# Kernel optimization log

Measured on AMD Instinct MI355X. Metric: run time of the kernel, lower is better.

The kernel has to match this reference:

```python
import jax, jax.numpy as jnp
import numpy as np

N_WIRES = 5
TOTAL = 2 * N_WIRES          # query branch simulates 2*n_wires qubits
DIM = 1 << TOTAL             # 1024
ENC = 1 << N_WIRES           # 32 = token encoder output dim


def setup_inputs() -> dict:
    key = jax.random.key(0)
    ks = jax.random.split(key, 6)
    B, T, C = 4, 32, 512
    x = jax.random.normal(ks[0], (B, T, C), jnp.float32)
    W_tok = jax.random.normal(ks[1], (ENC, C), jnp.float32) * 0.05
    b_tok = jax.random.normal(ks[2], (ENC,), jnp.float32) * 0.05
    theta_rx0 = jax.random.normal(ks[3], (TOTAL,), jnp.float32)
    theta_ry0 = jax.random.normal(ks[4], (TOTAL,), jnp.float32)
    theta_ry1 = jax.random.normal(ks[5], (TOTAL,), jnp.float32)
    return {"x": x, "W_tok": W_tok, "b_tok": b_tok,
            "theta_rx0": theta_rx0, "theta_ry0": theta_ry0, "theta_ry1": theta_ry1}


def _rx_mat(t):
    c = jnp.cos(t / 2).astype(jnp.complex64)
    s = jnp.sin(t / 2).astype(jnp.complex64)
    return jnp.stack([jnp.stack([c, -1j * s]), jnp.stack([-1j * s, c])])


def _ry_mat(t):
    c = jnp.cos(t / 2).astype(jnp.complex64)
    s = jnp.sin(t / 2).astype(jnp.complex64)
    return jnp.stack([jnp.stack([c, -s]), jnp.stack([s, c])])


def _apply_1q(state, U, w):
    # state: (bsz, 2, 2, ..., 2); wire w lives on axis 1+w (wire 0 = MSB)
    s = jnp.tensordot(state, U, axes=((1 + w,), (1,)))  # gate axis moves to last
    return jnp.moveaxis(s, -1, 1 + w)


def _apply_cnot(state, c, t):
    s = jnp.moveaxis(state, (1 + c, 1 + t), (-2, -1))
    s = s.at[..., 1, :].set(s[..., 1, ::-1])  # flip target where control == 1
    return jnp.moveaxis(s, (-2, -1), (1 + c, 1 + t))


def reference(x, W_tok, b_tok, theta_rx0, theta_ry0, theta_ry1):
    B, T, C = x.shape
    # token encoding + L2 normalize  -> (B, T, 32)
    enc = x @ W_tok.T + b_tok
    enc = enc / jnp.linalg.norm(enc, axis=-1, keepdims=True)
    # all T*T pairwise outer products, flattened as a_idx*32 + b_idx  -> (B, T*T, 1024)
    pairs = jnp.einsum('bip,bjq->bijpq', enc, enc).reshape(B, T * T, DIM)
    pairs = pairs / jnp.linalg.norm(pairs, axis=-1, keepdims=True)
    state = pairs.astype(jnp.complex64).reshape((B * T * T,) + (2,) * TOTAL)
    # layer 1: RX then RY on every wire
    for j in range(TOTAL):
        state = _apply_1q(state, _rx_mat(theta_rx0[j]), j)
        state = _apply_1q(state, _ry_mat(theta_ry0[j]), j)
    # CNOT ring
    for j in range(TOTAL):
        state = _apply_cnot(state, j, (j + 1) % TOTAL)
    # layer 2: RY on every wire
    for j in range(TOTAL):
        state = _apply_1q(state, _ry_mat(theta_ry1[j]), j)
    return state.reshape(B, T * T, DIM)
```

## Files before the change

### kernel.cpp

```cpp
#include <hip/hip_runtime.h>
#include <hip/hip_bf16.h>


typedef float vfloat4 __attribute__((ext_vector_type(4)));

__device__ __forceinline__ float2 shflx(float2 v, int mask) {
    return make_float2(__shfl_xor(v.x, mask, 64), __shfl_xor(v.y, mask, 64));
}

__global__ __launch_bounds__(256) void prep_kernel(const float* __restrict__ x,
                                                   const float* __restrict__ W,
                                                   const float* __restrict__ bt,
                                                   const float* __restrict__ rx0,
                                                   const float* __restrict__ ry0,
                                                   const float* __restrict__ ry1,
                                                   float2* __restrict__ U,
                                                   float2* __restrict__ V) {
    int row = blockIdx.x;
    int tid = threadIdx.x;

    __shared__ float g1[10][8];
    __shared__ float g2[10][2];
    __shared__ float esum[32];
    __shared__ float e[32];

    if (tid < 10) {
        float sx, cx, s0, c0, s1, c1;
        sincosf(rx0[tid] * 0.5f, &sx, &cx);
        sincosf(ry0[tid] * 0.5f, &s0, &c0);
        sincosf(ry1[tid] * 0.5f, &s1, &c1);
        g1[tid][0] = c0 * cx;  g1[tid][1] = s0 * sx;
        g1[tid][2] = -s0 * cx; g1[tid][3] = -c0 * sx;
        g1[tid][4] = s0 * cx;  g1[tid][5] = -c0 * sx;
        g1[tid][6] = c0 * cx;  g1[tid][7] = -s0 * sx;
        g2[tid][0] = c1;       g2[tid][1] = s1;
    }

    {
        int col = tid >> 3;
        int kk  = tid & 7;
        const float4* wp = (const float4*)(W + (size_t)col * 512 + kk * 4);
        const float4* xp = (const float4*)(x + (size_t)row * 512 + kk * 4);
        float acc = 0.f;
#pragma unroll
        for (int m = 0; m < 16; ++m) {
            float4 wv = wp[m * 8];
            float4 xv = xp[m * 8];
            acc += xv.x * wv.x + xv.y * wv.y + xv.z * wv.z + xv.w * wv.w;
        }
        acc += __shfl_xor(acc, 1, 64);
        acc += __shfl_xor(acc, 2, 64);
        acc += __shfl_xor(acc, 4, 64);
        if (kk == 0) esum[col] = acc;
    }
    __syncthreads();

    if (tid < 32) {
        float sum = esum[tid] + bt[tid];
        float sq = sum * sum;
#pragma unroll
        for (int off = 1; off < 32; off <<= 1) sq += __shfl_xor(sq, off, 64);
        e[tid] = sum * (1.0f / sqrtf(sq));
    }
    __syncthreads();

    {
        int grp = tid >> 5;
        int side = grp >> 2;
        int br = grp & 3;
        int s = br >> 1, t = br & 1;
        int p = tid & 31;
        int wb = side * 5;
        float2 c = make_float2(e[p], 0.f);
#pragma unroll
        for (int l = 0; l < 5; ++l) {
            int w = wb + l, bit = 1 << (4 - l);
            float2 pr = shflx(c, bit);
            float a0 = g1[w][0], a1 = g1[w][1], a2 = g1[w][2], a3 = g1[w][3];
            float a4 = g1[w][4], a5 = g1[w][5], a6 = g1[w][6], a7 = g1[w][7];
            float2 lo, hi;
            lo.x = a0 * c.x - a1 * c.y + a2 * pr.x - a3 * pr.y;
            lo.y = a0 * c.y + a1 * c.x + a2 * pr.y + a3 * pr.x;
            hi.x = a4 * pr.x - a5 * pr.y + a6 * c.x - a7 * c.y;
            hi.y = a4 * pr.y + a5 * pr.x + a6 * c.y + a7 * c.x;
            c = ((p & bit) == 0) ? lo : hi;
        }
        if (side == 0) {
#pragma unroll
            for (int l = 0; l < 4; ++l) {
                int cb = 1 << (4 - l), tb = 1 << (3 - l);
                float2 pr = shflx(c, tb);
                if (p & cb) c = pr;
            }
            if ((p & 1) != s) c = make_float2(0.f, 0.f);
            { float2 pr = shflx(c, 16); if (t) c = pr; }
        } else {
            { float2 pr = shflx(c, 16); if (s) c = pr; }
#pragma unroll
            for (int l = 0; l < 4; ++l) {
                int cb = 1 << (4 - l), tb = 1 << (3 - l);
                float2 pr = shflx(c, tb);
                if (p & cb) c = pr;
            }
            if ((p & 1) != t) c = make_float2(0.f, 0.f);
        }
#pragma unroll
        for (int l = 0; l < 5; ++l) {
            int w = wb + l, bit = 1 << (4 - l);
            float cy = g2[w][0], sy = g2[w][1];
            float2 pr = shflx(c, bit);
            c = ((p & bit) == 0)
                  ? make_float2(cy * c.x - sy * pr.x, cy * c.y - sy * pr.y)
                  : make_float2(sy * pr.x + cy * c.x, sy * pr.y + cy * c.y);
        }
        float2* dst = (side == 0) ? U : V;
        dst[(size_t)row * 128 + br * 32 + p] = c;
    }
}

__global__ __launch_bounds__(256) void outer_kernel(const float2* __restrict__ U,
                                                    const float2* __restrict__ V,
                                                    float* __restrict__ out,
                                                    int complex_out) {
    int bx = blockIdx.x;
    int b  = bx >> 8;
    int i  = (bx >> 3) & 31;
    int j0 = (bx & 7) * 4;
    int tid = threadIdx.x;

    __shared__ float2 su[128];
    __shared__ float2 sv[4][128];

    if (tid < 64)
        ((float4*)su)[tid] = ((const float4*)(U + (size_t)(b * 32 + i) * 128))[tid];
    ((float4*)sv)[tid] = ((const float4*)(V + (size_t)(b * 32 + j0) * 128))[tid];
    __syncthreads();

    int d0 = tid << 2;
    int pp = d0 >> 5;
    int q0 = d0 & 31;
    float2 up0 = su[pp], up1 = su[32 + pp], up2 = su[64 + pp], up3 = su[96 + pp];

#pragma unroll
    for (int jj = 0; jj < 4; ++jj) {
        const float2* svj = sv[jj];
        float2 acc[4];
#pragma unroll
        for (int ee = 0; ee < 4; ++ee) {
            int q = q0 + ee;
            float2 v0 = svj[q], v1 = svj[32 + q], v2 = svj[64 + q], v3 = svj[96 + q];
            float2 a;
            a.x = up0.x * v0.x - up0.y * v0.y + up1.x * v1.x - up1.y * v1.y
                + up2.x * v2.x - up2.y * v2.y + up3.x * v3.x - up3.y * v3.y;
            a.y = up0.x * v0.y + up0.y * v0.x + up1.x * v1.y + up1.y * v1.x
                + up2.x * v2.y + up2.y * v2.x + up3.x * v3.y + up3.y * v3.x;
            acc[ee] = a;
        }
        size_t pair = (size_t)b * 1024 + (size_t)i * 32 + (j0 + jj);
        if (complex_out) {
            vfloat4* o = (vfloat4*)(out + (pair * 1024 + d0) * 2);
            vfloat4 w0 = {acc[0].x, acc[0].y, acc[1].x, acc[1].y};
            vfloat4 w1 = {acc[2].x, acc[2].y, acc[3].x, acc[3].y};
            __builtin_nontemporal_store(w0, o);
            __builtin_nontemporal_store(w1, o + 1);
        } else {
            vfloat4* o = (vfloat4*)(out + pair * 1024 + d0);
            vfloat4 w0 = {acc[0].x, acc[1].x, acc[2].x, acc[3].x};
            __builtin_nontemporal_store(w0, o);
        }
    }
}

extern "C" void kernel_launch(void* const* d_in, const int* in_sizes, int n_in,
                              void* d_out, int out_size, void* d_ws, size_t ws_size,
                              hipStream_t stream) {
    const float* x   = (const float*)d_in[0];
    const float* W   = (const float*)d_in[1];
    const float* bt  = (const float*)d_in[2];
    const float* rx0 = (const float*)d_in[3];
    const float* ry0 = (const float*)d_in[4];
    const float* ry1 = (const float*)d_in[5];

    float2* U = (float2*)d_ws;
    float2* V = U + 16384;

    prep_kernel<<<128, 256, 0, stream>>>(x, W, bt, rx0, ry0, ry1, U, V);

    int complex_out = (out_size > 4 * 1024 * 1024) ? 1 : 0;
    outer_kernel<<<1024, 256, 0, stream>>>(U, V, (float*)d_out, complex_out);
}
```

Measured before the change: 74.94 us.

## Fuse token encoding and circuit prep into the outer-product kernel

Merges the prep kernel into the outer-product kernel. Each block now recomputes the token encodings and U/V factors for its own i row and four j rows, working in shared memory, so there is no workspace round-trip and only one launch. In exchange, every one of the 1024 blocks redoes the 5-row GEMV against W and the gate simulation. That is roughly 8x redundant compute and repeated W reads from cache.

```diff
diff --git a/kernel.cpp b/kernel.cpp
--- a/kernel.cpp
+++ b/kernel.cpp
@@ -1,5 +1,4 @@
 #include <hip/hip_runtime.h>
-#include <hip/hip_bf16.h>
 
 
 typedef float vfloat4 __attribute__((ext_vector_type(4)));
@@ -8,81 +7,116 @@
     return make_float2(__shfl_xor(v.x, mask, 64), __shfl_xor(v.y, mask, 64));
 }
 
-__global__ __launch_bounds__(256) void prep_kernel(const float* __restrict__ x,
-                                                   const float* __restrict__ W,
-                                                   const float* __restrict__ bt,
-                                                   const float* __restrict__ rx0,
-                                                   const float* __restrict__ ry0,
-                                                   const float* __restrict__ ry1,
-                                                   float2* __restrict__ U,
-                                                   float2* __restrict__ V) {
-    int row = blockIdx.x;
+__global__ __launch_bounds__(256) void fused_kernel(const float* __restrict__ x,
+                                                    const float* __restrict__ W,
+                                                    const float* __restrict__ bt,
+                                                    const float* __restrict__ rx0,
+                                                    const float* __restrict__ ry0,
+                                                    const float* __restrict__ ry1,
+                                                    float* __restrict__ out,
+                                                    int complex_out) {
+    int bx = blockIdx.x;
+    int b  = bx >> 8;
+    int i  = (bx >> 3) & 31;
+    int j0 = (bx & 7) * 4;
     int tid = threadIdx.x;
 
     __shared__ float g1[10][8];
     __shared__ float g2[10][2];
-    __shared__ float esum[32];
-    __shared__ float e[32];
+    __shared__ float sx[5][512];
+    __shared__ float eraw[5][32];
+    __shared__ float e[5][32];
+    __shared__ float2 su[128];
+    __shared__ float2 sv[4][128];
 
     if (tid < 10) {
-        float sx, cx, s0, c0, s1, c1;
-        sincosf(rx0[tid] * 0.5f, &sx, &cx);
+        float sxv, cxv, s0, c0, s1, c1;
+        sincosf(rx0[tid] * 0.5f, &sxv, &cxv);
         sincosf(ry0[tid] * 0.5f, &s0, &c0);
         sincosf(ry1[tid] * 0.5f, &s1, &c1);
-        g1[tid][0] = c0 * cx;  g1[tid][1] = s0 * sx;
-        g1[tid][2] = -s0 * cx; g1[tid][3] = -c0 * sx;
-        g1[tid][4] = s0 * cx;  g1[tid][5] = -c0 * sx;
-        g1[tid][6] = c0 * cx;  g1[tid][7] = -s0 * sx;
-        g2[tid][0] = c1;       g2[tid][1] = s1;
-    }
+        g1[tid][0] = c0 * cxv;  g1[tid][1] = s0 * sxv;
+        g1[tid][2] = -s0 * cxv; g1[tid][3] = -c0 * sxv;
+        g1[tid][4] = s0 * cxv;  g1[tid][5] = -c0 * sxv;
+        g1[tid][6] = c0 * cxv;  g1[tid][7] = -s0 * sxv;
+        g2[tid][0] = c1;        g2[tid][1] = s1;
+    }
+
+    {
+        const float4* xi = (const float4*)(x + (size_t)(b * 32 + i)  * 512);
+        const float4* xj = (const float4*)(x + (size_t)(b * 32 + j0) * 512);
+        if (tid < 128) ((float4*)&sx[0][0])[tid] = xi[tid];
+        float4* dj = (float4*)&sx[1][0];
+        dj[tid]       = xj[tid];
+        dj[tid + 256] = xj[tid + 256];
+    }
+    __syncthreads();
 
     {
         int col = tid >> 3;
         int kk  = tid & 7;
         const float4* wp = (const float4*)(W + (size_t)col * 512 + kk * 4);
-        const float4* xp = (const float4*)(x + (size_t)row * 512 + kk * 4);
-        float acc = 0.f;
+        float a0 = 0.f, a1 = 0.f, a2 = 0.f, a3 = 0.f, a4 = 0.f;
 #pragma unroll
         for (int m = 0; m < 16; ++m) {
             float4 wv = wp[m * 8];
-            float4 xv = xp[m * 8];
-            acc += xv.x * wv.x + xv.y * wv.y + xv.z * wv.z + xv.w * wv.w;
-        }
-        acc += __shfl_xor(acc, 1, 64);
-        acc += __shfl_xor(acc, 2, 64);
-        acc += __shfl_xor(acc, 4, 64);
-        if (kk == 0) esum[col] = acc;
-    }
-    __syncthreads();
-
-    if (tid < 32) {
-        float sum = esum[tid] + bt[tid];
+            int o = kk * 4 + m * 32;
+            float4 v0 = *(const float4*)&sx[0][o];
+            float4 v1 = *(const float4*)&sx[1][o];
+            float4 v2 = *(const float4*)&sx[2][o];
+            float4 v3 = *(const float4*)&sx[3][o];
+            float4 v4 = *(const float4*)&sx[4][o];
+            a0 += v0.x * wv.x + v0.y * wv.y + v0.z * wv.z + v0.w * wv.w;
+            a1 += v1.x * wv.x + v1.y * wv.y + v1.z * wv.z + v1.w * wv.w;
+            a2 += v2.x * wv.x + v2.y * wv.y + v2.z * wv.z + v2.w * wv.w;
+            a3 += v3.x * wv.x + v3.y * wv.y + v3.z * wv.z + v3.w * wv.w;
+            a4 += v4.x * wv.x + v4.y * wv.y + v4.z * wv.z + v4.w * wv.w;
+        }
+#pragma unroll
+        for (int mask = 1; mask <= 4; mask <<= 1) {
+            a0 += __shfl_xor(a0, mask, 64);
+            a1 += __shfl_xor(a1, mask, 64);
+            a2 += __shfl_xor(a2, mask, 64);
+            a3 += __shfl_xor(a3, mask, 64);
+            a4 += __shfl_xor(a4, mask, 64);
+        }
+        if (kk == 0) {
+            eraw[0][col] = a0; eraw[1][col] = a1; eraw[2][col] = a2;
+            eraw[3][col] = a3; eraw[4][col] = a4;
+        }
+    }
+    __syncthreads();
+
+    if (tid < 160) {
+        int r  = tid >> 5;
+        int cc = tid & 31;
+        float sum = eraw[r][cc] + bt[cc];
         float sq = sum * sum;
 #pragma unroll
-        for (int off = 1; off < 32; off <<= 1) sq += __shfl_xor(sq, off, 64);
-        e[tid] = sum * (1.0f / sqrtf(sq));
-    }
-    __syncthreads();
-
-    {
-        int grp = tid >> 5;
-        int side = grp >> 2;
-        int br = grp & 3;
+        for (int off = 1; off < 32; off <<= 1) sq += __shfl_xor(sq, off, 32);
+        e[r][cc] = sum * (1.0f / sqrtf(sq));
+    }
+    __syncthreads();
+
+    for (int g = tid >> 5; g < 20; g += 8) {
+        int side = (g >= 4) ? 1 : 0;
+        int q    = g - 4;
+        int br   = side ? (q & 3) : g;
+        int erow = side ? (1 + (q >> 2)) : 0;
         int s = br >> 1, t = br & 1;
         int p = tid & 31;
         int wb = side * 5;
-        float2 c = make_float2(e[p], 0.f);
+        float2 c = make_float2(e[erow][p], 0.f);
 #pragma unroll
         for (int l = 0; l < 5; ++l) {
             int w = wb + l, bit = 1 << (4 - l);
             float2 pr = shflx(c, bit);
-            float a0 = g1[w][0], a1 = g1[w][1], a2 = g1[w][2], a3 = g1[w][3];
-            float a4 = g1[w][4], a5 = g1[w][5], a6 = g1[w][6], a7 = g1[w][7];
+            float b0 = g1[w][0], b1 = g1[w][1], b2 = g1[w][2], b3 = g1[w][3];
+            float b4 = g1[w][4], b5 = g1[w][5], b6 = g1[w][6], b7 = g1[w][7];
             float2 lo, hi;
-            lo.x = a0 * c.x - a1 * c.y + a2 * pr.x - a3 * pr.y;
-            lo.y = a0 * c.y + a1 * c.x + a2 * pr.y + a3 * pr.x;
-            hi.x = a4 * pr.x - a5 * pr.y + a6 * c.x - a7 * c.y;
-            hi.y = a4 * pr.y + a5 * pr.x + a6 * c.y + a7 * c.x;
+            lo.x = b0 * c.x - b1 * c.y + b2 * pr.x - b3 * pr.y;
+            lo.y = b0 * c.y + b1 * c.x + b2 * pr.y + b3 * pr.x;
+            hi.x = b4 * pr.x - b5 * pr.y + b6 * c.x - b7 * c.y;
+            hi.y = b4 * pr.y + b5 * pr.x + b6 * c.y + b7 * c.x;
             c = ((p & bit) == 0) ? lo : hi;
         }
         if (side == 0) {
@@ -113,27 +147,9 @@
                   ? make_float2(cy * c.x - sy * pr.x, cy * c.y - sy * pr.y)
                   : make_float2(sy * pr.x + cy * c.x, sy * pr.y + cy * c.y);
         }
-        float2* dst = (side == 0) ? U : V;
-        dst[(size_t)row * 128 + br * 32 + p] = c;
-    }
-}
-
-__global__ __launch_bounds__(256) void outer_kernel(const float2* __restrict__ U,
-                                                    const float2* __restrict__ V,
-                                                    float* __restrict__ out,
-                                                    int complex_out) {
-    int bx = blockIdx.x;
-    int b  = bx >> 8;
-    int i  = (bx >> 3) & 31;
-    int j0 = (bx & 7) * 4;
-    int tid = threadIdx.x;
-
-    __shared__ float2 su[128];
-    __shared__ float2 sv[4][128];
-
-    if (tid < 64)
-        ((float4*)su)[tid] = ((const float4*)(U + (size_t)(b * 32 + i) * 128))[tid];
-    ((float4*)sv)[tid] = ((const float4*)(V + (size_t)(b * 32 + j0) * 128))[tid];
+        if (side == 0) su[br * 32 + p] = c;
+        else           sv[erow - 1][br * 32 + p] = c;
+    }
     __syncthreads();
 
     int d0 = tid << 2;
@@ -147,13 +163,13 @@
         float2 acc[4];
 #pragma unroll
         for (int ee = 0; ee < 4; ++ee) {
-            int q = q0 + ee;
-            float2 v0 = svj[q], v1 = svj[32 + q], v2 = svj[64 + q], v3 = svj[96 + q];
+            int qq = q0 + ee;
+            float2 w0 = svj[qq], w1 = svj[32 + qq], w2 = svj[64 + qq], w3 = svj[96 + qq];
             float2 a;
-            a.x = up0.x * v0.x - up0.y * v0.y + up1.x * v1.x - up1.y * v1.y
-                + up2.x * v2.x - up2.y * v2.y + up3.x * v3.x - up3.y * v3.y;
-            a.y = up0.x * v0.y + up0.y * v0.x + up1.x * v1.y + up1.y * v1.x
-                + up2.x * v2.y + up2.y * v2.x + up3.x * v3.y + up3.y * v3.x;
+            a.x = up0.x * w0.x - up0.y * w0.y + up1.x * w1.x - up1.y * w1.y
+                + up2.x * w2.x - up2.y * w2.y + up3.x * w3.x - up3.y * w3.y;
+            a.y = up0.x * w0.y + up0.y * w0.x + up1.x * w1.y + up1.y * w1.x
+                + up2.x * w2.y + up2.y * w2.x + up3.x * w3.y + up3.y * w3.x;
             acc[ee] = a;
         }
         size_t pair = (size_t)b * 1024 + (size_t)i * 32 + (j0 + jj);
@@ -181,11 +197,9 @@
     const float* ry0 = (const float*)d_in[4];
     const float* ry1 = (const float*)d_in[5];
 
-    float2* U = (float2*)d_ws;
-    float2* V = U + 16384;
-
-    prep_kernel<<<128, 256, 0, stream>>>(x, W, bt, rx0, ry0, ry1, U, V);
+    (void)d_ws; (void)ws_size;
 
     int complex_out = (out_size > 4 * 1024 * 1024) ? 1 : 0;
-    outer_kernel<<<1024, 256, 0, stream>>>(U, V, (float*)d_out, complex_out);
+    fused_kernel<<<1024, 256, 0, stream>>>(x, W, bt, rx0, ry0, ry1,
+                                           (float*)d_out, complex_out);
 }
```

After: 79.42 us. 1.06x slower.
